# Kernel optimization log

Measured on AMD Instinct MI355X. Metric: run time of the kernel, lower is better.

Reference implementation:

```python
import jax, jax.numpy as jnp
import numpy as np

VALUES_PER_ITEM = 4  # 2-bit packed -> 4 values per uint8


def setup_inputs() -> dict:
    key = jax.random.key(0)
    k1, k2, k3 = jax.random.split(key, 3)
    x = jax.random.normal(k1, (4, 4096, 2048), dtype=jnp.float32)
    # packed uint8 weights, stored as int32 with values in [0, 256)
    weight_packed = jax.random.randint(k2, (512, 2048), 0, 256, dtype=jnp.int32)
    weight_scale = jnp.ones((1,), dtype=jnp.float32)
    bias = jax.random.normal(k3, (2048,), dtype=jnp.float32) * 0.01
    return {"x": x, "weight_packed": weight_packed,
            "weight_scale": weight_scale, "bias": bias}


def unpack_weights_bitnet(packed, dtype):
    # packed: [out//4, in]. HF BitNet layout: group i occupies rows
    # [i*out//4 : (i+1)*out//4], extracted from bits (2i, 2i+1), minus 1.
    parts = [((packed >> (2 * i)) & 3) for i in range(VALUES_PER_ITEM)]
    return jnp.concatenate(parts, axis=0).astype(dtype) - 1.0  # [out, in]


def activation_quant(x, num_bits=8):
    qn = -(2 ** (num_bits - 1))          # -128
    qp = 2 ** (num_bits - 1) - 1         # 127
    amax = jnp.clip(jnp.max(jnp.abs(x), axis=-1, keepdims=True), 1e-5, None)
    scale = qp / amax                    # per-token scale, [..., 1]
    # round-half-to-even matches torch .round(); keep in float (int8-valued)
    xq = jnp.clip(jnp.round(x * scale), qn, qp)
    return xq, scale


def reference(x, weight_packed, weight_scale, bias):
    w = unpack_weights_bitnet(weight_packed, x.dtype)  # [out, in]
    xq, in_scale = activation_quant(x)                 # [b,s,in], [b,s,1]
    y = jnp.einsum('bsd,od->bso', xq, w)               # int8-valued GEMM in fp
    y = y / (weight_scale * in_scale)                  # rescale
    return y + bias
```

## Files before the change

kernel.cpp:

```cpp
#include <hip/hip_runtime.h>
#include <hip/hip_bf16.h>
#include <stdint.h>


typedef __attribute__((ext_vector_type(4))) int int4v;

#define GLOBAL_AS __attribute__((address_space(1)))
#define LDS_AS    __attribute__((address_space(3)))

static constexpr int MK = 2048;
static constexpr int NN = 2048;
static constexpr int MM = 16384;

__global__ void quant_kernel(const float* __restrict__ x,
                             const float* __restrict__ wscale,
                             signed char* __restrict__ xq,
                             float* __restrict__ rf) {
    const int m = blockIdx.x;
    const int t = threadIdx.x;
    const float4* xr = (const float4*)(x + (size_t)m * MK);
    float4 v0 = xr[t];
    float4 v1 = xr[t + 256];
    float amax = fmaxf(fmaxf(fabsf(v0.x), fabsf(v0.y)),
                       fmaxf(fabsf(v0.z), fabsf(v0.w)));
    amax = fmaxf(amax, fmaxf(fmaxf(fabsf(v1.x), fabsf(v1.y)),
                             fmaxf(fabsf(v1.z), fabsf(v1.w))));
    #pragma unroll
    for (int off = 32; off >= 1; off >>= 1)
        amax = fmaxf(amax, __shfl_xor(amax, off));
    __shared__ float smax[4];
    if ((t & 63) == 0) smax[t >> 6] = amax;
    __syncthreads();
    float a0 = fmaxf(fmaxf(smax[0], smax[1]), fmaxf(smax[2], smax[3]));
    a0 = fmaxf(a0, 1e-5f);
    const float scale = 127.0f / a0;
    if (t == 0) rf[m] = a0 / (127.0f * wscale[0]);

    auto q = [&](float f) -> int {
        float r = rintf(f * scale);
        r = fminf(fmaxf(r, -128.0f), 127.0f);
        return (int)r;
    };
    int p0 = (q(v0.x) & 255) | ((q(v0.y) & 255) << 8) |
             ((q(v0.z) & 255) << 16) | ((q(v0.w) & 255) << 24);
    int p1 = (q(v1.x) & 255) | ((q(v1.y) & 255) << 8) |
             ((q(v1.z) & 255) << 16) | ((q(v1.w) & 255) << 24);
    int* xqr = (int*)(xq + (size_t)m * MK);
    xqr[t]       = p0;
    xqr[t + 256] = p1;
}

__global__ void unpack_kernel(const int* __restrict__ packed,
                              signed char* __restrict__ W) {
    const int idx = blockIdx.x * 256 + threadIdx.x;
    const int r  = idx >> 9;
    const int kq = idx & 511;
    const int4 p = ((const int4*)packed)[idx];
    int* Wi = (int*)W;
    #pragma unroll
    for (int i = 0; i < 4; i++) {
        const int sh = 2 * i;
        int b0 = ((((p.x >> sh) & 3) - 1) & 255);
        int b1 = ((((p.y >> sh) & 3) - 1) & 255);
        int b2 = ((((p.z >> sh) & 3) - 1) & 255);
        int b3 = ((((p.w >> sh) & 3) - 1) & 255);
        Wi[(i * 512 + r) * 512 + kq] = b0 | (b1 << 8) | (b2 << 16) | (b3 << 24);
    }
}

__global__ void __launch_bounds__(256)
gemm_kernel(const signed char* __restrict__ xq,
            const signed char* __restrict__ W,
            const float* __restrict__ rf,
            const float* __restrict__ bias,
            float* __restrict__ out) {
    constexpr int BK = 64;
    __shared__ __attribute__((aligned(16))) unsigned char As[128 * BK];
    __shared__ __attribute__((aligned(16))) unsigned char Bs[128 * BK];

    const int tid  = threadIdx.x;
    const int wave = tid >> 6;
    const int lane = tid & 63;
    const int m0 = blockIdx.y * 128;
    const int n0 = blockIdx.x * 128;

    const int srow  = lane >> 2;
    const int sbyte = ((lane & 3) ^ ((srow >> 1) & 3)) * 16;

    const int wm = (wave >> 1) * 64;
    const int wn = (wave & 1) * 64;
    const int fr = lane & 15;
    const int fslot = ((lane >> 4) ^ ((fr >> 1) & 3)) * 16;

    int4v acc[4][4] = {};

    for (int k0 = 0; k0 < MK; k0 += BK) {
        #pragma unroll
        for (int c = 2 * wave; c < 2 * wave + 2; c++) {
            const signed char* ga =
                xq + (size_t)(m0 + c * 16 + srow) * MK + k0 + sbyte;
            __builtin_amdgcn_global_load_lds((const GLOBAL_AS void*)ga,
                                             (LDS_AS void*)(As + c * 1024),
                                             16, 0, 0);
            const signed char* gb =
                W + (size_t)(n0 + c * 16 + srow) * MK + k0 + sbyte;
            __builtin_amdgcn_global_load_lds((const GLOBAL_AS void*)gb,
                                             (LDS_AS void*)(Bs + c * 1024),
                                             16, 0, 0);
        }
        __syncthreads();

        int4v af[4], bf[4];
        #pragma unroll
        for (int i = 0; i < 4; i++) {
            af[i] = *(const int4v*)(As + (wm + i * 16 + fr) * BK + fslot);
            bf[i] = *(const int4v*)(Bs + (wn + i * 16 + fr) * BK + fslot);
        }
        #pragma unroll
        for (int mt = 0; mt < 4; mt++)
            #pragma unroll
            for (int nt = 0; nt < 4; nt++)
                acc[mt][nt] = __builtin_amdgcn_mfma_i32_16x16x64_i8(
                    af[mt], bf[nt], acc[mt][nt], 0, 0, 0);
        __syncthreads();
    }

    const int col   = lane & 15;
    const int rbase = (lane >> 4) * 4;
    #pragma unroll
    for (int mt = 0; mt < 4; mt++) {
        #pragma unroll
        for (int r = 0; r < 4; r++) {
            const int m = m0 + wm + mt * 16 + rbase + r;
            const float rfm = rf[m];
            #pragma unroll
            for (int nt = 0; nt < 4; nt++) {
                const int n = n0 + wn + nt * 16 + col;
                out[(size_t)m * NN + n] = (float)acc[mt][nt][r] * rfm + bias[n];
            }
        }
    }
}

extern "C" void kernel_launch(void* const* d_in, const int* in_sizes, int n_in,
                              void* d_out, int out_size, void* d_ws, size_t ws_size,
                              hipStream_t stream) {
    const float* x      = (const float*)d_in[0];
    const int*   packed = (const int*)d_in[1];
    const float* wscale = (const float*)d_in[2];
    const float* bias   = (const float*)d_in[3];
    float* out = (float*)d_out;

    signed char* xq = (signed char*)d_ws;
    signed char* W  = xq + (size_t)MM * MK;
    float*       rf = (float*)(W + (size_t)NN * MK);

    quant_kernel<<<MM, 256, 0, stream>>>(x, wscale, xq, rf);
    unpack_kernel<<<(512 * 512) / 256, 256, 0, stream>>>(packed, W);
    gemm_kernel<<<dim3(NN / 128, MM / 128), 256, 0, stream>>>(xq, W, rf, bias, out);
}
```

Measured before the change: 312.6 us.

## Double GEMM K-tile, swap grid order, and use wave-per-row quantization

The GEMM now stages a 128-byte K slice per iteration, using an 8-way XOR swizzle in LDS, which halves the number of barrier pairs per tile. The grid is transposed so that consecutive blocks walk along M and share the same weight columns. The quantization kernel is rewritten so that one wavefront handles a whole row with a grid-stride loop, which removes the LDS reduction and the block barrier. The changes bring larger LDS use per block and more registers held for x values in the quant kernel.

```diff
diff --git a/kernel.cpp b/kernel.cpp
--- a/kernel.cpp
+++ b/kernel.cpp
@@ -16,38 +16,43 @@
                              const float* __restrict__ wscale,
                              signed char* __restrict__ xq,
                              float* __restrict__ rf) {
-    const int m = blockIdx.x;
-    const int t = threadIdx.x;
-    const float4* xr = (const float4*)(x + (size_t)m * MK);
-    float4 v0 = xr[t];
-    float4 v1 = xr[t + 256];
-    float amax = fmaxf(fmaxf(fabsf(v0.x), fabsf(v0.y)),
-                       fmaxf(fabsf(v0.z), fabsf(v0.w)));
-    amax = fmaxf(amax, fmaxf(fmaxf(fabsf(v1.x), fabsf(v1.y)),
-                             fmaxf(fabsf(v1.z), fabsf(v1.w))));
-    #pragma unroll
-    for (int off = 32; off >= 1; off >>= 1)
-        amax = fmaxf(amax, __shfl_xor(amax, off));
-    __shared__ float smax[4];
-    if ((t & 63) == 0) smax[t >> 6] = amax;
-    __syncthreads();
-    float a0 = fmaxf(fmaxf(smax[0], smax[1]), fmaxf(smax[2], smax[3]));
-    a0 = fmaxf(a0, 1e-5f);
-    const float scale = 127.0f / a0;
-    if (t == 0) rf[m] = a0 / (127.0f * wscale[0]);
+    const int wv   = (blockIdx.x * 256 + threadIdx.x) >> 6;
+    const int lane = threadIdx.x & 63;
+    const float ws = wscale[0];
+    constexpr int NWAVES = 2048 * 256 / 64;
 
-    auto q = [&](float f) -> int {
-        float r = rintf(f * scale);
-        r = fminf(fmaxf(r, -128.0f), 127.0f);
-        return (int)r;
-    };
-    int p0 = (q(v0.x) & 255) | ((q(v0.y) & 255) << 8) |
-             ((q(v0.z) & 255) << 16) | ((q(v0.w) & 255) << 24);
-    int p1 = (q(v1.x) & 255) | ((q(v1.y) & 255) << 8) |
-             ((q(v1.z) & 255) << 16) | ((q(v1.w) & 255) << 24);
-    int* xqr = (int*)(xq + (size_t)m * MK);
-    xqr[t]       = p0;
-    xqr[t + 256] = p1;
+    for (int m = wv; m < MM; m += NWAVES) {
+        const float4* xr = (const float4*)(x + (size_t)m * MK);
+        float4 v[8];
+        #pragma unroll
+        for (int s = 0; s < 8; s++) v[s] = xr[s * 64 + lane];
+
+        float amax = 0.0f;
+        #pragma unroll
+        for (int s = 0; s < 8; s++)
+            amax = fmaxf(amax,
+                   fmaxf(fmaxf(fabsf(v[s].x), fabsf(v[s].y)),
+                         fmaxf(fabsf(v[s].z), fabsf(v[s].w))));
+        #pragma unroll
+        for (int off = 32; off >= 1; off >>= 1)
+            amax = fmaxf(amax, __shfl_xor(amax, off));
+        amax = fmaxf(amax, 1e-5f);
+        const float scale = 127.0f / amax;
+        if (lane == 0) rf[m] = amax / (127.0f * ws);
+
+        auto q = [&](float f) -> int {
+            float r = rintf(f * scale);
+            r = fminf(fmaxf(r, -128.0f), 127.0f);
+            return (int)r;
+        };
+        int* xqr = (int*)(xq + (size_t)m * MK);
+        #pragma unroll
+        for (int s = 0; s < 8; s++) {
+            int p = (q(v[s].x) & 255) | ((q(v[s].y) & 255) << 8) |
+                    ((q(v[s].z) & 255) << 16) | ((q(v[s].w) & 255) << 24);
+            xqr[s * 64 + lane] = p;
+        }
+    }
 }
 
 __global__ void unpack_kernel(const int* __restrict__ packed,
@@ -74,54 +79,59 @@
             const float* __restrict__ rf,
             const float* __restrict__ bias,
             float* __restrict__ out) {
-    constexpr int BK = 64;
+    constexpr int BK = 128;
     __shared__ __attribute__((aligned(16))) unsigned char As[128 * BK];
     __shared__ __attribute__((aligned(16))) unsigned char Bs[128 * BK];
 
     const int tid  = threadIdx.x;
     const int wave = tid >> 6;
     const int lane = tid & 63;
-    const int m0 = blockIdx.y * 128;
-    const int n0 = blockIdx.x * 128;
+    const int m0 = blockIdx.x * 128;
+    const int n0 = blockIdx.y * 128;
 
-    const int srow  = lane >> 2;
-    const int sbyte = ((lane & 3) ^ ((srow >> 1) & 3)) * 16;
+    const int srow  = lane >> 3;
+    const int sbyte = ((lane & 7) ^ (srow & 7)) * 16;
 
     const int wm = (wave >> 1) * 64;
     const int wn = (wave & 1) * 64;
     const int fr = lane & 15;
-    const int fslot = ((lane >> 4) ^ ((fr >> 1) & 3)) * 16;
+    const int fg = lane >> 4;
 
     int4v acc[4][4] = {};
 
     for (int k0 = 0; k0 < MK; k0 += BK) {
         #pragma unroll
-        for (int c = 2 * wave; c < 2 * wave + 2; c++) {
-            const signed char* ga =
-                xq + (size_t)(m0 + c * 16 + srow) * MK + k0 + sbyte;
+        for (int r = 0; r < 4; r++) {
+            const int row = r * 32 + wave * 8 + srow;
+            const signed char* ga = xq + (size_t)(m0 + row) * MK + k0 + sbyte;
             __builtin_amdgcn_global_load_lds((const GLOBAL_AS void*)ga,
-                                             (LDS_AS void*)(As + c * 1024),
+                                             (LDS_AS void*)(As + r * 4096 + wave * 1024),
                                              16, 0, 0);
-            const signed char* gb =
-                W + (size_t)(n0 + c * 16 + srow) * MK + k0 + sbyte;
+            const signed char* gb = W + (size_t)(n0 + row) * MK + k0 + sbyte;
             __builtin_amdgcn_global_load_lds((const GLOBAL_AS void*)gb,
-                                             (LDS_AS void*)(Bs + c * 1024),
+                                             (LDS_AS void*)(Bs + r * 4096 + wave * 1024),
                                              16, 0, 0);
         }
         __syncthreads();
 
-        int4v af[4], bf[4];
         #pragma unroll
-        for (int i = 0; i < 4; i++) {
-            af[i] = *(const int4v*)(As + (wm + i * 16 + fr) * BK + fslot);
-            bf[i] = *(const int4v*)(Bs + (wn + i * 16 + fr) * BK + fslot);
+        for (int ks = 0; ks < 2; ks++) {
+            const int c = ks * 4 + fg;
+            int4v af[4], bf[4];
+            #pragma unroll
+            for (int i = 0; i < 4; i++) {
+                const int ar = wm + i * 16 + fr;
+                af[i] = *(const int4v*)(As + ar * BK + (c ^ (ar & 7)) * 16);
+                const int br = wn + i * 16 + fr;
+                bf[i] = *(const int4v*)(Bs + br * BK + (c ^ (br & 7)) * 16);
+            }
+            #pragma unroll
+            for (int mt = 0; mt < 4; mt++)
+                #pragma unroll
+                for (int nt = 0; nt < 4; nt++)
+                    acc[mt][nt] = __builtin_amdgcn_mfma_i32_16x16x64_i8(
+                        af[mt], bf[nt], acc[mt][nt], 0, 0, 0);
         }
-        #pragma unroll
-        for (int mt = 0; mt < 4; mt++)
-            #pragma unroll
-            for (int nt = 0; nt < 4; nt++)
-                acc[mt][nt] = __builtin_amdgcn_mfma_i32_16x16x64_i8(
-                    af[mt], bf[nt], acc[mt][nt], 0, 0, 0);
         __syncthreads();
     }
 
@@ -155,7 +165,7 @@
     signed char* W  = xq + (size_t)MM * MK;
     float*       rf = (float*)(W + (size_t)NN * MK);
 
-    quant_kernel<<<MM, 256, 0, stream>>>(x, wscale, xq, rf);
+    quant_kernel<<<2048, 256, 0, stream>>>(x, wscale, xq, rf);
     unpack_kernel<<<(512 * 512) / 256, 256, 0, stream>>>(packed, W);
-    gemm_kernel<<<dim3(NN / 128, MM / 128), 256, 0, stream>>>(xq, W, rf, bias, out);
+    gemm_kernel<<<dim3(MM / 128, NN / 128), 256, 0, stream>>>(xq, W, rf, bias, out);
 }
```

Result: slower. 325.8 us (+4.2%).
